# Kernel tuning notes

Measured on AMD Instinct MI355X. Metric: run time of the kernel, lower is better.

Reference implementation:

```python
import jax, jax.numpy as jnp
import numpy as np

N = 1048576
D = 128
B = 4096


def setup_inputs() -> dict:
    key = jax.random.key(0)
    k_h, k_b, k_a, k_w, k_bias = jax.random.split(key, 5)
    h = jax.random.normal(k_h, (N, D), dtype=jnp.float32)
    batch_idx = jnp.sort(jax.random.randint(k_b, (N,), 0, B, dtype=jnp.int32))
    actions = jax.random.randint(k_a, (B,), 0, N, dtype=jnp.int32)
    node_mask = jnp.ones((N,), dtype=bool)
    # nn.Linear(D, 1) parameters
    W = jax.random.normal(k_w, (1, D), dtype=jnp.float32) / np.sqrt(D)
    b = jax.random.normal(k_bias, (1,), dtype=jnp.float32) * 0.01
    return {"actions": actions, "h": h, "batch_idx": batch_idx,
            "node_mask": node_mask, "n_graphs": B, "W": W, "b": b}


def reference(actions, h, batch_idx, node_mask, n_graphs, W, b):
    # node_logits = Linear(D -> 1)(h).squeeze()  -> [N]
    node_logits = (h @ W[0]) + b[0]
    neg_inf = jnp.float32(-1e30)
    masked = jnp.where(node_mask, node_logits, neg_inf)
    # per-graph (segment) softmax over nodes
    seg_max = jax.ops.segment_max(masked, batch_idx, num_segments=n_graphs)
    ex = jnp.where(node_mask, jnp.exp(masked - seg_max[batch_idx]), 0.0)
    seg_sum = jax.ops.segment_sum(ex, batch_idx, num_segments=n_graphs)
    p = ex / jnp.maximum(seg_sum[batch_idx], 1e-30)  # [N]
    # masked entropy per graph: -sum_{masked nodes} p log p
    safe_log = jnp.log(jnp.where(p > 0, p, 1.0))
    plogp = jnp.where(node_mask, p * safe_log, 0.0)
    entropy = -jax.ops.segment_sum(plogp, batch_idx, num_segments=n_graphs)  # [B]
    logprob = jnp.log(p[actions])  # [B]
    return (logprob, entropy)
```

## Files before the change

### kernel.cpp

```cpp
#include <hip/hip_runtime.h>
#include <hip/hip_bf16.h>
#include <cmath>


typedef float f32x4 __attribute__((ext_vector_type(4)));

__device__ __forceinline__ f32x4 nt_load4(const float* p) {
    return __builtin_nontemporal_load(reinterpret_cast<const f32x4*>(p));
}

__global__ __launch_bounds__(256) void k_action(
    const float* __restrict__ h, const float* __restrict__ W,
    const float* __restrict__ bvec, const int* __restrict__ actions,
    float* __restrict__ xa, int B)
{
    const int lane = threadIdx.x & 63;
    const int sub = lane >> 4;
    const int sl = lane & 15;
    int g = (blockIdx.x * (blockDim.x >> 6) + (threadIdx.x >> 6)) * 4 + sub;
    if (g >= B) return;

    const f32x4 wA = *reinterpret_cast<const f32x4*>(W + sl * 4);
    const f32x4 wB = *reinterpret_cast<const f32x4*>(W + 64 + sl * 4);

    long a = actions[g];
    const float* hp = h + a * 128;
    const f32x4 v0 = *reinterpret_cast<const f32x4*>(hp + sl * 4);
    const f32x4 v1 = *reinterpret_cast<const f32x4*>(hp + 64 + sl * 4);
    float part = v0.x * wA.x + v0.y * wA.y + v0.z * wA.z + v0.w * wA.w +
                 v1.x * wB.x + v1.y * wB.y + v1.z * wB.z + v1.w * wB.w;
#pragma unroll
    for (int off = 8; off; off >>= 1)
        part += __shfl_xor(part, off, 16);
    if (sl == 0) xa[g] = part + bvec[0];
}

__global__ __launch_bounds__(256) void k_main(
    const float* __restrict__ h, const float* __restrict__ W,
    const float* __restrict__ bvec, const int* __restrict__ bidx,
    const int* __restrict__ mask,
    float* __restrict__ S, float* __restrict__ T, int N, int rows_per_wave)
{
    const int lane = threadIdx.x & 63;
    const int sub = lane >> 4;
    const int sl = lane & 15;
    const int wave = blockIdx.x * (blockDim.x >> 6) + (threadIdx.x >> 6);
    long r0 = (long)wave * rows_per_wave;
    if (r0 >= N) return;
    long r1 = r0 + rows_per_wave;
    if (r1 > N) r1 = N;

    const f32x4 wA = *reinterpret_cast<const f32x4*>(W + sl * 4);
    const f32x4 wB = *reinterpret_cast<const f32x4*>(W + 64 + sl * 4);
    const float bb = bvec[0];

    int curSeg = -1;
    float eS = 0.0f, eT = 0.0f;

#pragma unroll 8
    for (long r = r0 + sub; r < r1; r += 4) {
        const float* hp = h + r * 128;
        const f32x4 a = nt_load4(hp + sl * 4);
        const f32x4 c = nt_load4(hp + 64 + sl * 4);
        float part = a.x * wA.x + a.y * wA.y + a.z * wA.z + a.w * wA.w +
                     c.x * wB.x + c.y * wB.y + c.z * wB.z + c.w * wB.w;
#pragma unroll
        for (int off = 8; off; off >>= 1)
            part += __shfl_xor(part, off, 16);
        float x = part + bb;
        if (sl == 0) {
            float e = 0.0f, ex = 0.0f;
            if (__builtin_nontemporal_load(mask + r)) {
                e = __expf(x);
                ex = e * x;
            }
            int seg = __builtin_nontemporal_load(bidx + r);
            if (seg != curSeg) {
                if (curSeg >= 0) {
                    atomicAdd(&S[curSeg], eS);
                    atomicAdd(&T[curSeg], eT);
                }
                curSeg = seg;
                eS = e;
                eT = ex;
            } else {
                eS += e;
                eT += ex;
            }
        }
    }
    if (curSeg >= 0) {
        atomicAdd(&S[curSeg], eS);
        atomicAdd(&T[curSeg], eT);
    }
}

__global__ void k_final(
    const float* __restrict__ xa, const int* __restrict__ bidx,
    const int* __restrict__ mask, const int* __restrict__ actions,
    const float* __restrict__ S, const float* __restrict__ T,
    float* __restrict__ out, int B)
{
    int g = blockIdx.x * blockDim.x + threadIdx.x;
    if (g >= B) return;

    float s = S[g];
    float ent = 0.0f;
    if (s > 0.0f) ent = logf(s) - T[g] / s;
    out[B + g] = ent;

    int a = actions[g];
    int ga = bidx[a];
    float sa = fmaxf(S[ga], 1e-30f);
    float lp = mask[a] ? (xa[g] - logf(sa)) : -INFINITY;
    out[g] = lp;
}

extern "C" void kernel_launch(void* const* d_in, const int* in_sizes, int n_in,
                              void* d_out, int out_size, void* d_ws,
                              size_t ws_size, hipStream_t stream) {
    const int* actions = (const int*)d_in[0];
    const float* h = (const float*)d_in[1];
    const int* bidx = (const int*)d_in[2];
    const int* mask = (const int*)d_in[3];
    const float* W = (const float*)d_in[5];
    const float* bias = (const float*)d_in[6];
    float* out = (float*)d_out;

    const int B = out_size / 2;
    const int N = in_sizes[2];

    float* S = (float*)d_ws;
    float* T = S + B;
    float* xa = T + B;

    hipMemsetAsync(S, 0, (size_t)2 * B * sizeof(float), stream);

    int ablocks = (B + 15) / 16;
    k_action<<<ablocks, 256, 0, stream>>>(h, W, bias, actions, xa, B);

    const int ROWS_PER_WAVE = 128;
    int waves = (N + ROWS_PER_WAVE - 1) / ROWS_PER_WAVE;
    int blocks = (waves + 3) / 4;
    k_main<<<blocks, 256, 0, stream>>>(h, W, bias, bidx, mask, S, T, N,
                                       ROWS_PER_WAVE);

    k_final<<<(B + 255) / 256, 256, 0, stream>>>(xa, bidx, mask, actions, S, T,
                                                 out, B);
}
```

Measured before the change: 106.7 us.

## Fuse action, main and final kernels into one launch with last-block finalize

Merges the three kernels into a single grid. Extra blocks compute the action logits, and the last block to finish, found through an atomic counter, computes the entropy and logprob outputs. This removes two kernel launches and the gaps between them. The cost is a grid-wide atomic counter, thread fences, and a serial finalize step run by one 256-thread block over B graphs.

Result: slower. 265.5 us (+148.8%).

```diff
diff --git a/kernel.cpp b/kernel.cpp
--- a/kernel.cpp
+++ b/kernel.cpp
@@ -9,111 +9,113 @@
     return __builtin_nontemporal_load(reinterpret_cast<const f32x4*>(p));
 }
 
-__global__ __launch_bounds__(256) void k_action(
+__global__ __launch_bounds__(256) void k_fused(
     const float* __restrict__ h, const float* __restrict__ W,
-    const float* __restrict__ bvec, const int* __restrict__ actions,
-    float* __restrict__ xa, int B)
+    const float* __restrict__ bvec, const int* __restrict__ bidx,
+    const int* __restrict__ mask, const int* __restrict__ actions,
+    float* S, float* T, float* xa, unsigned* ctr, float* out,
+    int N, int B, int rows_per_wave, int mblocks)
 {
     const int lane = threadIdx.x & 63;
     const int sub = lane >> 4;
     const int sl = lane & 15;
-    int g = (blockIdx.x * (blockDim.x >> 6) + (threadIdx.x >> 6)) * 4 + sub;
-    if (g >= B) return;
-
-    const f32x4 wA = *reinterpret_cast<const f32x4*>(W + sl * 4);
-    const f32x4 wB = *reinterpret_cast<const f32x4*>(W + 64 + sl * 4);
-
-    long a = actions[g];
-    const float* hp = h + a * 128;
-    const f32x4 v0 = *reinterpret_cast<const f32x4*>(hp + sl * 4);
-    const f32x4 v1 = *reinterpret_cast<const f32x4*>(hp + 64 + sl * 4);
-    float part = v0.x * wA.x + v0.y * wA.y + v0.z * wA.z + v0.w * wA.w +
-                 v1.x * wB.x + v1.y * wB.y + v1.z * wB.z + v1.w * wB.w;
-#pragma unroll
-    for (int off = 8; off; off >>= 1)
-        part += __shfl_xor(part, off, 16);
-    if (sl == 0) xa[g] = part + bvec[0];
-}
-
-__global__ __launch_bounds__(256) void k_main(
-    const float* __restrict__ h, const float* __restrict__ W,
-    const float* __restrict__ bvec, const int* __restrict__ bidx,
-    const int* __restrict__ mask,
-    float* __restrict__ S, float* __restrict__ T, int N, int rows_per_wave)
-{
-    const int lane = threadIdx.x & 63;
-    const int sub = lane >> 4;
-    const int sl = lane & 15;
-    const int wave = blockIdx.x * (blockDim.x >> 6) + (threadIdx.x >> 6);
-    long r0 = (long)wave * rows_per_wave;
-    if (r0 >= N) return;
-    long r1 = r0 + rows_per_wave;
-    if (r1 > N) r1 = N;
+    const int wv = threadIdx.x >> 6;
 
     const f32x4 wA = *reinterpret_cast<const f32x4*>(W + sl * 4);
     const f32x4 wB = *reinterpret_cast<const f32x4*>(W + 64 + sl * 4);
     const float bb = bvec[0];
 
-    int curSeg = -1;
-    float eS = 0.0f, eT = 0.0f;
+    if (blockIdx.x < mblocks) {
+        const int wave = blockIdx.x * 4 + wv;
+        long r0 = (long)wave * rows_per_wave;
+        long r1 = r0 + rows_per_wave;
+        if (r1 > N) r1 = N;
+
+        int curSeg = -1;
+        float eS = 0.0f, eT = 0.0f;
 
 #pragma unroll 8
-    for (long r = r0 + sub; r < r1; r += 4) {
-        const float* hp = h + r * 128;
-        const f32x4 a = nt_load4(hp + sl * 4);
-        const f32x4 c = nt_load4(hp + 64 + sl * 4);
-        float part = a.x * wA.x + a.y * wA.y + a.z * wA.z + a.w * wA.w +
-                     c.x * wB.x + c.y * wB.y + c.z * wB.z + c.w * wB.w;
+        for (long r = r0 + sub; r < r1; r += 4) {
+            const float* hp = h + r * 128;
+            const f32x4 a = nt_load4(hp + sl * 4);
+            const f32x4 c = nt_load4(hp + 64 + sl * 4);
+            float part = a.x * wA.x + a.y * wA.y + a.z * wA.z + a.w * wA.w +
+                         c.x * wB.x + c.y * wB.y + c.z * wB.z + c.w * wB.w;
 #pragma unroll
-        for (int off = 8; off; off >>= 1)
-            part += __shfl_xor(part, off, 16);
-        float x = part + bb;
-        if (sl == 0) {
-            float e = 0.0f, ex = 0.0f;
-            if (__builtin_nontemporal_load(mask + r)) {
-                e = __expf(x);
-                ex = e * x;
-            }
-            int seg = __builtin_nontemporal_load(bidx + r);
-            if (seg != curSeg) {
-                if (curSeg >= 0) {
-                    atomicAdd(&S[curSeg], eS);
-                    atomicAdd(&T[curSeg], eT);
+            for (int off = 8; off; off >>= 1)
+                part += __shfl_xor(part, off, 16);
+            float x = part + bb;
+            if (sl == 0) {
+                float e = 0.0f, ex = 0.0f;
+                if (__builtin_nontemporal_load(mask + r)) {
+                    e = __expf(x);
+                    ex = e * x;
                 }
-                curSeg = seg;
-                eS = e;
-                eT = ex;
-            } else {
-                eS += e;
-                eT += ex;
+                int seg = __builtin_nontemporal_load(bidx + r);
+                if (seg != curSeg) {
+                    if (curSeg >= 0) {
+                        atomicAdd(&S[curSeg], eS);
+                        atomicAdd(&T[curSeg], eT);
+                    }
+                    curSeg = seg;
+                    eS = e;
+                    eT = ex;
+                } else {
+                    eS += e;
+                    eT += ex;
+                }
             }
         }
+        if (curSeg >= 0) {
+            atomicAdd(&S[curSeg], eS);
+            atomicAdd(&T[curSeg], eT);
+        }
+    } else {
+        int g = (blockIdx.x - mblocks) * 16 + wv * 4 + sub;
+        if (g < B) {
+            long a = actions[g];
+            const float* hp = h + a * 128;
+            const f32x4 v0 = *reinterpret_cast<const f32x4*>(hp + sl * 4);
+            const f32x4 v1 = *reinterpret_cast<const f32x4*>(hp + 64 + sl * 4);
+            float part = v0.x * wA.x + v0.y * wA.y + v0.z * wA.z + v0.w * wA.w +
+                         v1.x * wB.x + v1.y * wB.y + v1.z * wB.z + v1.w * wB.w;
+#pragma unroll
+            for (int off = 8; off; off >>= 1)
+                part += __shfl_xor(part, off, 16);
+            if (sl == 0)
+                __hip_atomic_store(xa + g, part + bb, __ATOMIC_RELAXED,
+                                   __HIP_MEMORY_SCOPE_AGENT);
+        }
     }
-    if (curSeg >= 0) {
-        atomicAdd(&S[curSeg], eS);
-        atomicAdd(&T[curSeg], eT);
+
+    __shared__ bool isLast;
+    __syncthreads();
+    if (threadIdx.x == 0) {
+        __threadfence();
+        unsigned old = __hip_atomic_fetch_add(ctr, 1u, __ATOMIC_ACQ_REL,
+                                              __HIP_MEMORY_SCOPE_AGENT);
+        isLast = (old == (unsigned)(gridDim.x - 1));
     }
-}
+    __syncthreads();
+    if (!isLast) return;
 
-__global__ void k_final(
-    const float* __restrict__ xa, const int* __restrict__ bidx,
-    const int* __restrict__ mask, const int* __restrict__ actions,
-    const float* __restrict__ S, const float* __restrict__ T,
-    float* __restrict__ out, int B)
-{
-    int g = blockIdx.x * blockDim.x + threadIdx.x;
-    if (g >= B) return;
+    __threadfence();
+    for (int g = threadIdx.x; g < B; g += blockDim.x) {
+        float s = __hip_atomic_load(S + g, __ATOMIC_RELAXED,
+                                    __HIP_MEMORY_SCOPE_AGENT);
+        float t = __hip_atomic_load(T + g, __ATOMIC_RELAXED,
+                                    __HIP_MEMORY_SCOPE_AGENT);
+        out[B + g] = (s > 0.0f) ? (logf(s) - t / s) : 0.0f;
 
-    float s = S[g];
-    float ent = 0.0f;
-    if (s > 0.0f) ent = logf(s) - T[g] / s;
-    out[B + g] = ent;
-
-    int a = actions[g];
-    int ga = bidx[a];
-    float sa = fmaxf(S[ga], 1e-30f);
-    float lp = mask[a] ? (xa[g] - logf(sa)) : -INFINITY;
-    out[g] = lp;
+        int a = actions[g];
+        int ga = bidx[a];
+        float sg = __hip_atomic_load(S + ga, __ATOMIC_RELAXED,
+                                     __HIP_MEMORY_SCOPE_AGENT);
+        float xg = __hip_atomic_load(xa + g, __ATOMIC_RELAXED,
+                                     __HIP_MEMORY_SCOPE_AGENT);
+        float lp = mask[a] ? (xg - logf(fmaxf(sg, 1e-30f))) : -INFINITY;
+        out[g] = lp;
+    }
 }
 
 extern "C" void kernel_launch(void* const* d_in, const int* in_sizes, int n_in,
@@ -132,19 +134,16 @@
 
     float* S = (float*)d_ws;
     float* T = S + B;
-    float* xa = T + B;
+    unsigned* ctr = (unsigned*)(T + B);
+    float* xa = (float*)(T + B + 4);
 
-    hipMemsetAsync(S, 0, (size_t)2 * B * sizeof(float), stream);
-
-    int ablocks = (B + 15) / 16;
-    k_action<<<ablocks, 256, 0, stream>>>(h, W, bias, actions, xa, B);
+    hipMemsetAsync(S, 0, (size_t)(2 * B + 1) * sizeof(float), stream);
 
     const int ROWS_PER_WAVE = 128;
     int waves = (N + ROWS_PER_WAVE - 1) / ROWS_PER_WAVE;
-    int blocks = (waves + 3) / 4;
-    k_main<<<blocks, 256, 0, stream>>>(h, W, bias, bidx, mask, S, T, N,
-                                       ROWS_PER_WAVE);
-
-    k_final<<<(B + 255) / 256, 256, 0, stream>>>(xa, bidx, mask, actions, S, T,
-                                                 out, B);
+    int mblocks = (waves + 3) / 4;
+    int ablocks = (B + 15) / 16;
+    k_fused<<<mblocks + ablocks, 256, 0, stream>>>(
+        h, W, bias, bidx, mask, actions, S, T, xa, ctr, out, N, B,
+        ROWS_PER_WAVE, mblocks);
 }
```
